# Kernel tuning notes

Hardware: AMD Instinct MI355X
Metric: run time of the kernel (lower is better)

## Reference

```python
import jax, jax.numpy as jnp
import numpy as np

HS_LIST = [1024, 2048]   # hidden_size choices
IS_LIST = [2752, 5504]   # intermediate_size choices
A_BITS = [4, 8]
W_BITS = [4, 8]


def fake_quant(t, bits):
    # symmetric per-tensor fake quantization with straight-through estimator
    qmax = 2.0 ** (bits - 1) - 1.0
    s = jnp.maximum(jnp.max(jnp.abs(t)) / qmax, 1e-8)
    q = jnp.round(t / s) * s
    return t + jax.lax.stop_gradient(q - t)


def mixed_linear(inp, W, in_sizes, out_sizes, p_in, p_out, p_a, p_w):
    """Weight-entangled mixed-precision linear: weighted sum over the
    cartesian product of (in_size, out_size, a_bit, w_bit) choices.
    W has shape [max(out_sizes), max(in_sizes)]; sub-slices are shared."""
    out_max = max(out_sizes)
    acc = jnp.zeros(inp.shape[:-1] + (out_max,), inp.dtype)
    for i, cin in enumerate(in_sizes):
        x_sub = inp[..., :cin]
        for k, ab in enumerate(A_BITS):
            xq = fake_quant(x_sub, ab)
            for j, cout in enumerate(out_sizes):
                w_sub = W[:cout, :cin]
                for l, wb in enumerate(W_BITS):
                    wq = fake_quant(w_sub, wb)
                    y = jnp.einsum('bsh,oh->bso', xq, wq)
                    y = jnp.pad(y, ((0, 0), (0, 0), (0, out_max - cout)))
                    acc = acc + (p_in[i] * p_out[j] * p_a[k] * p_w[l]) * y
    return acc


def setup_inputs() -> dict:
    key = jax.random.key(0)
    ks = jax.random.split(key, 8)
    HS, IS = max(HS_LIST), max(IS_LIST)
    return {
        'x': jax.random.normal(ks[0], (1, 1024, HS), jnp.float32),
        'p_hidden': jax.random.normal(ks[1], (2,), jnp.float32),
        'p_inter': jax.random.normal(ks[2], (2,), jnp.float32),
        'p_abit': jax.random.normal(ks[3], (2,), jnp.float32),
        'p_wbit': jax.random.normal(ks[4], (2,), jnp.float32),
        'W_gate': jax.random.normal(ks[5], (IS, HS), jnp.float32) * 0.02,
        'W_up': jax.random.normal(ks[6], (IS, HS), jnp.float32) * 0.02,
        'W_down': jax.random.normal(ks[7], (HS, IS), jnp.float32) * 0.02,
    }


def reference(x, p_hidden, p_inter, p_abit, p_wbit, W_gate, W_up, W_down):
    # mixop softmaxes the architecture parameters into mixture probabilities
    wh = jax.nn.softmax(p_hidden)
    wi = jax.nn.softmax(p_inter)
    wa = jax.nn.softmax(p_abit)
    ww = jax.nn.softmax(p_wbit)
    x_up = mixed_linear(x, W_up, HS_LIST, IS_LIST, wh, wi, wa, ww)
    x_gate = jax.nn.silu(mixed_linear(x, W_gate, HS_LIST, IS_LIST, wh, wi, wa, ww))
    h = x_gate * x_up
    # down_proj (reverse=True): input dims are intermediate, output dims hidden;
    # op list is built over (intermediate, hidden) choices, weighted in the same
    # arch-param order (hidden probs pair with the first/intermediate choice axis).
    out = mixed_linear(h, W_down, IS_LIST, HS_LIST, wh, wi, wa, ww)
    return out
```

## Files before the change

kernel.cpp:

```cpp
#include <hip/hip_runtime.h>

typedef __attribute__((ext_vector_type(8))) short short8;
typedef __attribute__((ext_vector_type(4))) float f32x4;
typedef unsigned short u16;
typedef unsigned int u32;
typedef unsigned long long u64;

#define P_WH 0
#define P_WI 2
#define P_WA 4
#define P_WW 6
#define SL_AX 8
#define SL_WUP 12
#define SL_WGATE 16
#define SL_WDOWN 20
#define SL_AH 24
#define P_SX 28
#define P_SWUP 32
#define P_SWGATE 40
#define P_SWDOWN 48
#define P_SH 56

__device__ __forceinline__ u16 f2bf(float f) {
  u32 u = __float_as_uint(f);
  u = (u + 0x7FFFu + ((u >> 16) & 1u)) >> 16;
  return (u16)u;
}
__device__ __forceinline__ float bf2f(u16 h) { return __uint_as_float(((u32)h) << 16); }
__device__ __forceinline__ float fquant(float v, float s) { return rintf(v / s) * s; }

typedef const __attribute__((address_space(1))) u32 gl_u32;
typedef __attribute__((address_space(3))) u32 lds_u32;
__device__ __forceinline__ void gload_lds16(const void* g, void* l) {
  __builtin_amdgcn_global_load_lds((gl_u32*)g, (lds_u32*)l, 16, 0, 0);
}

#define WAITVM8()  asm volatile("s_waitcnt vmcnt(8)" ::: "memory")
#define WAITVM2()  asm volatile("s_waitcnt vmcnt(2)" ::: "memory")
#define WAITVM0()  asm volatile("s_waitcnt vmcnt(0)" ::: "memory")
#define BARRIER()  asm volatile("s_barrier" ::: "memory")

__global__ void k_init(const float* ph, const float* pi, const float* pa,
                       const float* pw, float* P) {
  if (threadIdx.x == 0) {
    u32* U = (u32*)P;
    for (int i = SL_AX; i < SL_AH + 2; ++i) U[i] = 0u;
    const float* src[4] = {ph, pi, pa, pw};
    #pragma unroll
    for (int t = 0; t < 4; ++t) {
      float a = src[t][0], b = src[t][1];
      float mx = fmaxf(a, b);
      float ea = expf(a - mx), eb = expf(b - mx);
      float s = ea + eb;
      P[t * 2 + 0] = ea / s;
      P[t * 2 + 1] = eb / s;
    }
  }
}

template <bool POW2>
__device__ __forceinline__ void amax_proc(float4 d, int v, u32 magic, int C,
                                          int r0, int c0,
                                          float& m0, float& m1, float& m2, float& m3) {
  int lin = v << 2;
  int o, c;
  if (POW2) { o = lin >> 11; c = lin & 2047; }
  else {
    o = (int)(((u64)(u32)lin * magic) >> 40);
    c = lin - o * C;
  }
  float mm = fmaxf(fmaxf(fabsf(d.x), fabsf(d.y)), fmaxf(fabsf(d.z), fabsf(d.w)));
  bool rlo = o < r0, clo = c < c0;
  m0 = fmaxf(m0, (rlo && clo) ? mm : 0.f);
  m1 = fmaxf(m1, (rlo && !clo) ? mm : 0.f);
  m2 = fmaxf(m2, (!rlo && clo) ? mm : 0.f);
  m3 = fmaxf(m3, (!rlo && !clo) ? mm : 0.f);
}

template <bool POW2>
__device__ __forceinline__ void absmax_dev(const float4* __restrict__ A4,
                                           int nvec, u32 magic, int C, int r0, int c0,
                                           int slotbase, float* P, int bid, int nb) {
  float m0 = 0.f, m1 = 0.f, m2 = 0.f, m3 = 0.f;
  const int tid = threadIdx.x;
  const int step = nb * 256;
  int v = bid * 256 + tid;
  for (; v + 3 * step < nvec; v += 4 * step) {
    float4 d0 = A4[v];
    float4 d1 = A4[v + step];
    float4 d2 = A4[v + 2 * step];
    float4 d3 = A4[v + 3 * step];
    amax_proc<POW2>(d0, v,            magic, C, r0, c0, m0, m1, m2, m3);
    amax_proc<POW2>(d1, v + step,     magic, C, r0, c0, m0, m1, m2, m3);
    amax_proc<POW2>(d2, v + 2 * step, magic, C, r0, c0, m0, m1, m2, m3);
    amax_proc<POW2>(d3, v + 3 * step, magic, C, r0, c0, m0, m1, m2, m3);
  }
  for (; v < nvec; v += step) {
    float4 d0 = A4[v];
    amax_proc<POW2>(d0, v, magic, C, r0, c0, m0, m1, m2, m3);
  }
  #pragma unroll
  for (int off = 32; off > 0; off >>= 1) {
    m0 = fmaxf(m0, __shfl_xor(m0, off));
    m1 = fmaxf(m1, __shfl_xor(m1, off));
    m2 = fmaxf(m2, __shfl_xor(m2, off));
    m3 = fmaxf(m3, __shfl_xor(m3, off));
  }
  __shared__ float red[16];
  const int wave = tid >> 6;
  if ((tid & 63) == 0) {
    red[wave * 4 + 0] = m0;
    red[wave * 4 + 1] = m1;
    red[wave * 4 + 2] = m2;
    red[wave * 4 + 3] = m3;
  }
  __syncthreads();
  if (tid < 4) {
    float mm = fmaxf(fmaxf(red[tid], red[4 + tid]), fmaxf(red[8 + tid], red[12 + tid]));
    if (mm > 0.f) atomicMax((u32*)P + slotbase + tid, __float_as_uint(mm));
  }
}

__global__ __launch_bounds__(256) void k_absmax4(const float* x, const float* Wu,
                                                 const float* Wg, const float* Wd,
                                                 u32 magic5504, float* P) {
  int b = blockIdx.x;
  if (b < 256)        absmax_dev<true >((const float4*)x,  (1024 * 2048) >> 2, 0, 2048, 1024, 1024, SL_AX,    P, b,        256);
  else if (b < 768)   absmax_dev<true >((const float4*)Wu, (5504 * 2048) >> 2, 0, 2048, 2752, 1024, SL_WUP,   P, b - 256,  512);
  else if (b < 1280)  absmax_dev<true >((const float4*)Wg, (5504 * 2048) >> 2, 0, 2048, 2752, 1024, SL_WGATE, P, b - 768,  512);
  else                absmax_dev<false>((const float4*)Wd, (2048 * 5504) >> 2, magic5504, 5504, 1024, 2752, SL_WDOWN, P, b - 1280, 512);
}

__global__ void k_params1(float* P) {
  if (threadIdx.x != 0 || blockIdx.x != 0) return;
  u32* U = (u32*)P;
  float x00 = __uint_as_float(U[SL_AX + 0]);
  float x01 = __uint_as_float(U[SL_AX + 1]);
  float ax0 = x00;
  float ax1 = fmaxf(x00, x01);
  P[P_SX + 0] = fmaxf(ax0 / 7.f, 1e-8f);
  P[P_SX + 1] = fmaxf(ax0 / 127.f, 1e-8f);
  P[P_SX + 2] = fmaxf(ax1 / 7.f, 1e-8f);
  P[P_SX + 3] = fmaxf(ax1 / 127.f, 1e-8f);
  const int sl[3] = {SL_WUP, SL_WGATE, SL_WDOWN};
  const int sb[3] = {P_SWUP, P_SWGATE, P_SWDOWN};
  #pragma unroll
  for (int t = 0; t < 3; ++t) {
    float q00 = __uint_as_float(U[sl[t] + 0]);
    float q01 = __uint_as_float(U[sl[t] + 1]);
    float q10 = __uint_as_float(U[sl[t] + 2]);
    float q11 = __uint_as_float(U[sl[t] + 3]);
    float a0 = q00;
    float a1 = fmaxf(q00, q10);
    float a2 = fmaxf(q00, q01);
    float a3 = fmaxf(fmaxf(q00, q01), fmaxf(q10, q11));
    float aa[4] = {a0, a1, a2, a3};
    #pragma unroll
    for (int ij = 0; ij < 4; ++ij) {
      P[sb[t] + ij * 2 + 0] = fmaxf(aa[ij] / 7.f, 1e-8f);
      P[sb[t] + ij * 2 + 1] = fmaxf(aa[ij] / 127.f, 1e-8f);
    }
  }
}

__global__ void k_params2(float* P) {
  if (threadIdx.x != 0 || blockIdx.x != 0) return;
  u32* U = (u32*)P;
  float a0 = __uint_as_float(U[SL_AH]);
  float a1 = fmaxf(a0, __uint_as_float(U[SL_AH + 1]));
  P[P_SH + 0] = fmaxf(a0 / 7.f, 1e-8f);
  P[P_SH + 1] = fmaxf(a0 / 127.f, 1e-8f);
  P[P_SH + 2] = fmaxf(a1 / 7.f, 1e-8f);
  P[P_SH + 3] = fmaxf(a1 / 127.f, 1e-8f);
}

__device__ __forceinline__ void build_x_one(
    const float* __restrict__ src, const float* __restrict__ P,
    u16* __restrict__ Xh, u16* __restrict__ Xl,
    int Csrc, int cin0, int K, int sbx, int gid, int kpr) {
  int row = gid / kpr;
  int kc_out = (gid - row * kpr) << 3;
  int kc_log = kc_out ^ (((row >> 1) & 3) << 3);
  int i = (kc_log >= cin0) ? 1 : 0;
  int c = kc_log - i * cin0;
  float pin = P[P_WH + i];
  float wa0 = P[P_WA], wa1 = P[P_WA + 1];
  float s4 = P[sbx + i * 2], s8 = P[sbx + i * 2 + 1];
  const float* sp = src + (size_t)row * Csrc + c;
  float v[8];
  *(float4*)&v[0] = *(const float4*)sp;
  *(float4*)&v[4] = *(const float4*)(sp + 4);
  short8 hv, lv;
  #pragma unroll
  for (int e = 0; e < 8; ++e) {
    float val = pin * (wa0 * fquant(v[e], s4) + wa1 * fquant(v[e], s8));
    u16 h = f2bf(val);
    hv[e] = (short)h;
    lv[e] = (short)f2bf(val - bf2f(h));
  }
  size_t off = (size_t)row * K + kc_out;
  *(short8*)(Xh + off) = hv;
  *(short8*)(Xl + off) = lv;
}

__device__ __forceinline__ void build_w_one(
    const float* __restrict__ W, const float* __restrict__ P,
    u16* __restrict__ Wh, u16* __restrict__ Wl,
    int Csrc, int cin0, int K, int sbw, int cout0,
    int row_src, int row_store, int kc_out) {
  int kc_log = kc_out ^ (((row_store >> 1) & 3) << 3);
  int i = (kc_log >= cin0) ? 1 : 0;
  int c = kc_log - i * cin0;
  float wi0 = P[P_WI], wi1 = P[P_WI + 1];
  float ww0 = P[P_WW], ww1 = P[P_WW + 1];
  float s00 = P[sbw + i * 4 + 0];
  float s01 = P[sbw + i * 4 + 1];
  float s10 = P[sbw + i * 4 + 2];
  float s11 = P[sbw + i * 4 + 3];
  float keep0 = (row_src < cout0) ? wi0 : 0.f;
  const float* sp = W + (size_t)row_src * Csrc + c;
  float v[8];
  *(float4*)&v[0] = *(const float4*)sp;
  *(float4*)&v[4] = *(const float4*)(sp + 4);
  short8 hv, lv;
  #pragma unroll
  for (int e = 0; e < 8; ++e) {
    float w = v[e];
    float t0 = ww0 * fquant(w, s00) + ww1 * fquant(w, s01);
    float t1 = ww0 * fquant(w, s10) + ww1 * fquant(w, s11);
    float val = keep0 * t0 + wi1 * t1;
    u16 h = f2bf(val);
    hv[e] = (short)h;
    lv[e] = (short)f2bf(val - bf2f(h));
  }
  size_t off = (size_t)row_store * K + kc_out;
  *(short8*)(Wh + off) = hv;
  *(short8*)(Wl + off) = lv;
}

__global__ __launch_bounds__(256) void k_build_x(
    const float* __restrict__ src, const float* __restrict__ P,
    u16* __restrict__ Xh, u16* __restrict__ Xl,
    int rows, int Csrc, int cin0, int K, int sbx) {
  int kpr = K >> 3;
  int nch = rows * kpr;
  int gid = blockIdx.x * blockDim.x + threadIdx.x;
  if (gid >= nch) return;
  build_x_one(src, P, Xh, Xl, Csrc, cin0, K, sbx, gid, kpr);
}

__global__ __launch_bounds__(256) void k_build_w(
    const float* __restrict__ W, const float* __restrict__ P,
    u16* __restrict__ Wh, u16* __restrict__ Wl,
    int R, int Csrc, int cin0, int K, int sbw, int cout0) {
  int kpr = K >> 3;
  int nch = R * kpr;
  int gid = blockIdx.x * blockDim.x + threadIdx.x;
  if (gid >= nch) return;
  int row = gid / kpr;
  int kc_out = (gid - row * kpr) << 3;
  build_w_one(W, P, Wh, Wl, Csrc, cin0, K, sbw, cout0, row, row, kc_out);
}

__global__ __launch_bounds__(256) void k_build1(
    const float* __restrict__ x, const float* __restrict__ Wu,
    const float* __restrict__ Wg, const float* __restrict__ P,
    u16* __restrict__ X1h, u16* __restrict__ X1l,
    u16* __restrict__ Wh, u16* __restrict__ Wl) {
  int bid = blockIdx.x;
  if (bid < 1536) {
    int gid = bid * 256 + threadIdx.x;
    build_x_one(x, P, X1h, X1l, 2048, 1024, 3072, P_SX, gid, 384);
  } else {
    int gid = (bid - 1536) * 256 + threadIdx.x;
    const int nch = 5504 * 384;
    bool isg = gid >= nch;
    int g2 = isg ? gid - nch : gid;
    int row = g2 / 384;
    int kc_out = (g2 - row * 384) << 3;
    int row_store = (((row >> 4) << 5) + (row & 15)) + (isg ? 16 : 0);
    if (!isg)
      build_w_one(Wu, P, Wh, Wl, 2048, 1024, 3072, P_SWUP,   2752, row, row_store, kc_out);
    else
      build_w_one(Wg, P, Wh, Wl, 2048, 1024, 3072, P_SWGATE, 2752, row, row_store, kc_out);
  }
}

__global__ __launch_bounds__(256) void k_build2(
    const float* __restrict__ H, const float* __restrict__ Wd,
    const float* __restrict__ P,
    u16* __restrict__ X2h, u16* __restrict__ X2l,
    u16* __restrict__ Wdh, u16* __restrict__ Wdl) {
  int bid = blockIdx.x;
  if (bid < 4128) {
    int gid = bid * 256 + threadIdx.x;
    build_x_one(H, P, X2h, X2l, 5504, 2752, 8256, P_SH, gid, 1032);
  } else {
    int gid = (bid - 4128) * 256 + threadIdx.x;
    int row = gid / 1032;
    int kc_out = (gid - row * 1032) << 3;
    build_w_one(Wd, P, Wdh, Wdl, 5504, 2752, 8256, P_SWDOWN, 1024, row, row, kc_out);
  }
}

__global__ __launch_bounds__(256) void k_h(const float* __restrict__ U_,
                                           const float* __restrict__ G_,
                                           float* __restrict__ H_, float* P) {
  int nvec = (1024 * 5504) >> 2;
  int gstride = gridDim.x * blockDim.x;
  float m0 = 0.f, m1 = 0.f;
  for (int v = blockIdx.x * blockDim.x + threadIdx.x; v < nvec; v += gstride) {
    float4 u = ((const float4*)U_)[v];
    float4 g = ((const float4*)G_)[v];
    float4 h;
    h.x = u.x * (g.x / (1.f + expf(-g.x)));
    h.y = u.y * (g.y / (1.f + expf(-g.y)));
    h.z = u.z * (g.z / (1.f + expf(-g.z)));
    h.w = u.w * (g.w / (1.f + expf(-g.w)));
    ((float4*)H_)[v] = h;
    int c = (v << 2) % 5504;
    float mm = fmaxf(fmaxf(fabsf(h.x), fabsf(h.y)), fmaxf(fabsf(h.z), fabsf(h.w)));
    if (c < 2752) m0 = fmaxf(m0, mm); else m1 = fmaxf(m1, mm);
  }
  #pragma unroll
  for (int off = 32; off > 0; off >>= 1) {
    m0 = fmaxf(m0, __shfl_xor(m0, off));
    m1 = fmaxf(m1, __shfl_xor(m1, off));
  }
  if ((threadIdx.x & 63) == 0) {
    u32* slots = (u32*)P;
    if (m0 > 0.f) atomicMax(slots + SL_AH, __float_as_uint(m0));
    if (m1 > 0.f) atomicMax(slots + SL_AH + 1, __float_as_uint(m1));
  }
}

template <int MF, int NF>
__global__ __launch_bounds__(256) void k_gemm(
    const u16* __restrict__ Ah, const u16* __restrict__ Al,
    const u16* __restrict__ Bh, const u16* __restrict__ Bl,
    float* __restrict__ C0, float* __restrict__ C1, int nsplit, int ldc,
    int M, int N, int K) {
  constexpr int BM = MF * 32;
  constexpr int BN = NF * 32;
  constexpr int HALF = (2 * BM + 2 * BN) * 32;
  constexpr int nsegA = BM / 16;
  constexpr int nsegB = BN / 16;
  constexpr int NSEG = 2 * nsegA + 2 * nsegB;
  constexpr int NJ = NSEG / 4;
  static_assert(NJ == 8, "vmcnt immediates assume 8 loads per stage");
  __shared__ __align__(16) u16 S[2 * HALF];

  const int tid = threadIdx.x;
  const int wave = tid >> 6;
  const int lane = tid & 63;

  const int gx = gridDim.x;
  const int nwg = gx * gridDim.y;
  const int orig = blockIdx.y * gx + blockIdx.x;
  const int q = nwg >> 3, r = nwg & 7;
  const int xcd = orig & 7, linb = orig >> 3;
  const int swz = (xcd < r ? xcd * (q + 1) : r * (q + 1) + (xcd - r) * q) + linb;
  const int m0 = (swz % gx) * BM;
  const int n0 = (swz / gx) * BN;

  const int St = K >> 5;
  const int Z = gridDim.z;
  const int zb = St / Z, zr = St - zb * Z;
  const int z = blockIdx.z;
  const int nst = zb + ((z < zr) ? 1 : 0);
  const int k0 = (z * zb + ((z < zr) ? z : zr)) << 5;

  const int wr = wave >> 1, wc = wave & 1;
  const int lrow = lane >> 2;
  const int lcol = (lane & 3) << 3;
  const int fr = lane & 15;
  const int fq4 = (lane >> 4) << 2;
  const int kofs = (lane >> 4) << 3;

  f32x4 acc[MF][NF];
  #pragma unroll
  for (int m = 0; m < MF; ++m)
    #pragma unroll
    for (int n = 0; n < NF; ++n) acc[m][n] = (f32x4){0.f, 0.f, 0.f, 0.f};

  const u16* srcp[NJ];
  int loff[NJ];
  #pragma unroll
  for (int j = 0; j < NJ; ++j) {
    int g = j * 4 + wave;
    const u16* gb; int abase, trow, segi;
    if (g < nsegA)               { gb = Ah; abase = 0;                  trow = m0; segi = g; }
    else if (g < 2 * nsegA)      { gb = Al; abase = BM * 32;            trow = m0; segi = g - nsegA; }
    else if (g < 2 * nsegA + nsegB) { gb = Bh; abase = 2 * BM * 32;     trow = n0; segi = g - 2 * nsegA; }
    else                         { gb = Bl; abase = 2 * BM * 32 + BN * 32; trow = n0; segi = g - 2 * nsegA - nsegB; }
    srcp[j] = gb + (size_t)(trow + segi * 16 + lrow) * K + (k0 + lcol);
    loff[j] = abase + segi * 512;
  }

  int aoh[MF], aol[MF], boh[NF], bol[NF];
  #pragma unroll
  for (int m = 0; m < MF; ++m) {
    int rr = wr * (MF * 16) + m * 16 + fr;
    int idx = rr * 32 + (kofs ^ (((rr >> 1) & 3) << 3));
    aoh[m] = idx;
    aol[m] = BM * 32 + idx;
  }
  #pragma unroll
  for (int n = 0; n < NF; ++n) {
    int rr = wc * (NF * 16) + n * 16 + fr;
    int idx = rr * 32 + (kofs ^ (((rr >> 1) & 3) << 3));
    boh[n] = 2 * BM * 32 + idx;
    bol[n] = 2 * BM * 32 + BN * 32 + idx;
  }

  #define STAGE(bufo)                                           \
    { _Pragma("unroll")                                         \
      for (int j = 0; j < NJ; ++j) {                            \
        gload_lds16(srcp[j], S + (bufo) + loff[j]);             \
        srcp[j] += 32;                                          \
      } }

  #define COMPUTE(bufo)                                                         \
    { short8 afh[MF], afl[MF], bfh[NF], bfl[NF];                                \
      _Pragma("unroll")                                                         \
      for (int m = 0; m < MF; ++m) {                                            \
        afh[m] = *(const short8*)(S + (bufo) + aoh[m]);                         \
        afl[m] = *(const short8*)(S + (bufo) + aol[m]);                         \
      }                                                                         \
      _Pragma("unroll")                                                         \
      for (int n = 0; n < NF; ++n) {                                            \
        bfh[n] = *(const short8*)(S + (bufo) + boh[n]);                         \
        bfl[n] = *(const short8*)(S + (bufo) + bol[n]);                         \
      }                                                                         \
      _Pragma("unroll")                                                         \
      for (int m = 0; m < MF; ++m)                                              \
        _Pragma("unroll")                                                       \
        for (int n = 0; n < NF; ++n) {                                          \
          acc[m][n] = __builtin_amdgcn_mfma_f32_16x16x32_bf16(afh[m], bfh[n], acc[m][n], 0, 0, 0); \
          acc[m][n] = __builtin_amdgcn_mfma_f32_16x16x32_bf16(afh[m], bfl[n], acc[m][n], 0, 0, 0); \
          acc[m][n] = __builtin_amdgcn_mfma_f32_16x16x32_bf16(afl[m], bfh[n], acc[m][n], 0, 0, 0); \
        } }

  int curo = 0;
  STAGE(curo);
  for (int t = 0; t + 1 < nst; ++t) {
    STAGE(curo ^ HALF);
    WAITVM8();
    BARRIER();
    COMPUTE(curo);
    BARRIER();
    curo ^= HALF;
  }
  WAITVM0();
  BARRIER();
  COMPUTE(curo);

  #undef STAGE
  #undef COMPUTE

  float* base = (n0 < nsplit) ? C0 : C1;
  const int ncol0 = (n0 < nsplit) ? 0 : nsplit;
  float* Cz = base + (size_t)z * M * ldc;
  #pragma unroll
  for (int m = 0; m < MF; ++m) {
    #pragma unroll
    for (int n = 0; n < NF; ++n) {
      int row = m0 + wr * (MF * 16) + m * 16 + fq4;
      int col = n0 + wc * (NF * 16) + n * 16 + fr - ncol0;
      float* cp = Cz + (size_t)row * ldc + col;
      f32x4 a = acc[m][n];
      cp[0] = a[0];
      cp[(size_t)ldc] = a[1];
      cp[(size_t)2 * ldc] = a[2];
      cp[(size_t)3 * ldc] = a[3];
    }
  }
}

template <int CMODE>
__global__ __launch_bounds__(512) void k_gemm8w(
    const u16* __restrict__ Ah, const u16* __restrict__ Al,
    const u16* __restrict__ Bh, const u16* __restrict__ Bl,
    float* __restrict__ C0, float* __restrict__ C1, int nsplit, int ldc,
    int M, int N, int K) {
  constexpr int BM = 256, BN = 256;
  constexpr int HALF = (2 * BM + 2 * BN) * 32;
  constexpr int NJ = 8;
  __shared__ __align__(16) u16 S[2 * HALF];

  const int tid = threadIdx.x;
  const int wave = tid >> 6;
  const int lane = tid & 63;

  const int gx = gridDim.x;
  const int nwg = gx * gridDim.y;
  const int orig = blockIdx.y * gx + blockIdx.x;
  const int q = nwg >> 3, r = nwg & 7;
  const int xcd = orig & 7, linb = orig >> 3;
  const int swz = (xcd < r ? xcd * (q + 1) : r * (q + 1) + (xcd - r) * q) + linb;
  const int m0 = (swz % gx) * BM;
  const int n0 = (swz / gx) * BN;

  const int St = K >> 5;
  const int Z = gridDim.z;
  const int zb = St / Z, zr = St - zb * Z;
  const int z = blockIdx.z;
  const int nst = zb + ((z < zr) ? 1 : 0);
  const int k0 = (z * zb + ((z < zr) ? z : zr)) << 5;

  const int wr = wave >> 2;
  const int wc = wave & 3;
  const int lrow = lane >> 2;
  const int lcol = (lane & 3) << 3;
  const int fr = lane & 15;
  const int fq4 = (lane >> 4) << 2;
  const int kofs = (lane >> 4) << 3;
  const int kx = kofs ^ (((fr >> 1) & 3) << 3);

  f32x4 acc[8][4];
  #pragma unroll
  for (int m = 0; m < 8; ++m)
    #pragma unroll
    for (int n = 0; n < 4; ++n) acc[m][n] = (f32x4){0.f, 0.f, 0.f, 0.f};

  const u16* srcp[NJ];
  int loff[NJ];
  #pragma unroll
  for (int j = 0; j < NJ; ++j) {
    int g = j * 8 + wave;
    const u16* gb; int abase, trow, segi;
    if (g < 16)      { gb = Ah; abase = 0;         trow = m0; segi = g; }
    else if (g < 32) { gb = Al; abase = 8192;      trow = m0; segi = g - 16; }
    else if (g < 48) { gb = Bh; abase = 16384;     trow = n0; segi = g - 32; }
    else             { gb = Bl; abase = 24576;     trow = n0; segi = g - 48; }
    srcp[j] = gb + (size_t)(trow + segi * 16 + lrow) * K + (k0 + lcol);
    loff[j] = abase + segi * 512;
  }

  const int aoh0 = (wr * 128 + fr) * 32 + kx;
  const int aol0 = 8192 + aoh0;
  const int boh0 = 16384 + (wc * 64 + fr) * 32 + kx;
  const int bol0 = boh0 + 8192;

  #define ISSUE2(bufo, j0)                                             \
    { gload_lds16(srcp[j0], S + (bufo) + loff[j0]);  srcp[j0] += 32;   \
      gload_lds16(srcp[j0+1], S + (bufo) + loff[j0+1]); srcp[j0+1] += 32; }

  int curo = 0;
  ISSUE2(curo, 0); ISSUE2(curo, 2); ISSUE2(curo, 4); ISSUE2(curo, 6);

  for (int t = 0; t < nst; ++t) {
    const int nxt = curo ^ HALF;
    const bool more = (t + 1 < nst);
    if (more) { ISSUE2(nxt, 0); WAITVM2(); } else { WAITVM0(); }
    BARRIER();

    short8 bh_[4], bl_[4];
    #pragma unroll
    for (int p = 0; p < 4; ++p) {
      const int m2 = 2 * p;
      short8 a0h = *(const short8*)(S + curo + aoh0 + m2 * 512);
      short8 a0l = *(const short8*)(S + curo + aol0 + m2 * 512);
      short8 a1h = *(const short8*)(S + curo + aoh0 + (m2 + 1) * 512);
      short8 a1l = *(const short8*)(S + curo + aol0 + (m2 + 1) * 512);
      if (p == 0) {
        #pragma unroll
        for (int n = 0; n < 4; ++n) {
          bh_[n] = *(const short8*)(S + curo + boh0 + n * 512);
          bl_[n] = *(const short8*)(S + curo + bol0 + n * 512);
        }
      }
      if (more) {
        if (p == 0) { ISSUE2(nxt, 2); }
        else if (p == 1) { ISSUE2(nxt, 4); }
        else if (p == 2) { ISSUE2(nxt, 6); }
      }
      BARRIER();
      __builtin_amdgcn_s_setprio(1);
      #pragma unroll
      for (int n = 0; n < 4; ++n) {
        acc[m2][n] = __builtin_amdgcn_mfma_f32_16x16x32_bf16(a0h, bh_[n], acc[m2][n], 0, 0, 0);
        acc[m2][n] = __builtin_amdgcn_mfma_f32_16x16x32_bf16(a0h, bl_[n], acc[m2][n], 0, 0, 0);
        acc[m2][n] = __builtin_amdgcn_mfma_f32_16x16x32_bf16(a0l, bh_[n], acc[m2][n], 0, 0, 0);
        acc[m2+1][n] = __builtin_amdgcn_mfma_f32_16x16x32_bf16(a1h, bh_[n], acc[m2+1][n], 0, 0, 0);
        acc[m2+1][n] = __builtin_amdgcn_mfma_f32_16x16x32_bf16(a1h, bl_[n], acc[m2+1][n], 0, 0, 0);
        acc[m2+1][n] = __builtin_amdgcn_mfma_f32_16x16x32_bf16(a1l, bh_[n], acc[m2+1][n], 0, 0, 0);
      }
      __builtin_amdgcn_s_setprio(0);
      BARRIER();
    }
    curo ^= HALF;
  }
  #undef ISSUE2

  if (CMODE == 2) {
    float hm0 = 0.f, hm1 = 0.f;
    #pragma unroll
    for (int nn = 0; nn < 2; ++nn) {
      const int n = nn * 2;
      int lcol2 = (((n0 + wc * 64 + n * 16) >> 5) << 4) + fr;
      bool lo = lcol2 < 2752;
      #pragma unroll
      for (int m = 0; m < 8; ++m) {
        int row = m0 + wr * 128 + m * 16 + fq4;
        float* hp = C0 + (size_t)row * ldc + lcol2;
        f32x4 au = acc[m][n], ag = acc[m][n + 1];
        #pragma unroll
        for (int j = 0; j < 4; ++j) {
          float g = ag[j];
          float h = au[j] * (g / (1.f + expf(-g)));
          hp[(size_t)j * ldc] = h;
          float a = fabsf(h);
          if (lo) hm0 = fmaxf(hm0, a); else hm1 = fmaxf(hm1, a);
        }
      }
    }
    #pragma unroll
    for (int off = 32; off > 0; off >>= 1) {
      hm0 = fmaxf(hm0, __shfl_xor(hm0, off));
      hm1 = fmaxf(hm1, __shfl_xor(hm1, off));
    }
    if (lane == 0) {
      u32* slots = (u32*)C1;
      if (hm0 > 0.f) atomicMax(slots + SL_AH, __float_as_uint(hm0));
      if (hm1 > 0.f) atomicMax(slots + SL_AH + 1, __float_as_uint(hm1));
    }
  } else {
    float* Cz = (z < 4) ? (C0 + (size_t)z * M * ldc) : (C1 + (size_t)(z - 4) * M * ldc);
    #pragma unroll
    for (int m = 0; m < 8; ++m) {
      #pragma unroll
      for (int n = 0; n < 4; ++n) {
        int row = m0 + wr * 128 + m * 16 + fq4;
        int col = n0 + wc * 64 + n * 16 + fr;
        float* cp = Cz + (size_t)row * ldc + col;
        f32x4 a = acc[m][n];
        cp[0] = a[0];
        cp[(size_t)ldc] = a[1];
        cp[(size_t)2 * ldc] = a[2];
        cp[(size_t)3 * ldc] = a[3];
      }
    }
  }
}

__global__ __launch_bounds__(256) void k_reduce8(const float4* __restrict__ p0,
                                                 const float4* __restrict__ p1,
                                                 float4* __restrict__ out, int nvec) {
  int stride = gridDim.x * blockDim.x;
  for (int i = blockIdx.x * blockDim.x + threadIdx.x; i < nvec; i += stride) {
    float4 s = p0[i];
    #pragma unroll
    for (int zz = 1; zz < 4; ++zz) {
      float4 b = p0[(size_t)zz * nvec + i];
      s.x += b.x; s.y += b.y; s.z += b.z; s.w += b.w;
    }
    #pragma unroll
    for (int zz = 0; zz < 4; ++zz) {
      float4 b = p1[(size_t)zz * nvec + i];
      s.x += b.x; s.y += b.y; s.z += b.z; s.w += b.w;
    }
    out[i] = s;
  }
}

__global__ __launch_bounds__(256) void k_reduce4(const float4* __restrict__ p,
                                                 float4* __restrict__ out, int nvec) {
  int stride = gridDim.x * blockDim.x;
  for (int i = blockIdx.x * blockDim.x + threadIdx.x; i < nvec; i += stride) {
    float4 a = p[i], b = p[nvec + i], c = p[2 * nvec + i], d = p[3 * nvec + i];
    float4 o;
    o.x = ((a.x + b.x) + c.x) + d.x;
    o.y = ((a.y + b.y) + c.y) + d.y;
    o.z = ((a.z + b.z) + c.z) + d.z;
    o.w = ((a.w + b.w) + c.w) + d.w;
    out[i] = o;
  }
}

extern "C" void kernel_launch(void* const* d_in, const int* in_sizes, int n_in,
                              void* d_out, int out_size, void* d_ws, size_t ws_size,
                              hipStream_t stream) {
  const float* x  = (const float*)d_in[0];
  const float* ph = (const float*)d_in[1];
  const float* pi = (const float*)d_in[2];
  const float* pa = (const float*)d_in[3];
  const float* pw = (const float*)d_in[4];
  const float* Wg = (const float*)d_in[5];
  const float* Wu = (const float*)d_in[6];
  const float* Wd = (const float*)d_in[7];
  float* out = (float*)d_out;

  const u32 magic5504 = (u32)(((1ULL << 40) + 5503ULL) / 5504ULL);
  char* ws = (char*)d_ws;

  const size_t szX1 = (size_t)1024 * 3072 * 2;
  const size_t szWug = (size_t)11008 * 3072 * 2;
  const size_t szH = (size_t)1024 * 5504 * 4;
  const size_t szDP = (size_t)4 * 1024 * 2048 * 4;
  const size_t fused_need = 1024 + 2 * szX1 + 2 * szWug + szH + szDP;

  if (ws_size >= fused_need) {
    size_t off = 0;
    float* P = (float*)(ws + off); off += 1024;
    u16* X1h = (u16*)(ws + off); off += szX1;
    u16* X1l = (u16*)(ws + off); off += szX1;
    u16* Wh  = (u16*)(ws + off); off += szWug;
    u16* Wl  = (u16*)(ws + off); off += szWug;
    float* H = (float*)(ws + off); off += szH;
    float* DPz0 = (float*)(ws + off); off += szDP;
    u16* X2h = Wh;
    u16* X2l = Wh + (size_t)1024 * 8256;
    float* DPz1 = (float*)(Wh + (size_t)2 * 1024 * 8256);
    u16* Wdh = Wl;
    u16* Wdl = Wl + (size_t)2048 * 8256;

    k_init<<<1, 64, 0, stream>>>(ph, pi, pa, pw, P);
    k_absmax4<<<1792, 256, 0, stream>>>(x, Wu, Wg, Wd, magic5504, P);
    k_params1<<<1, 64, 0, stream>>>(P);

    k_build1<<<1536 + 16512, 256, 0, stream>>>(x, Wu, Wg, P, X1h, X1l, Wh, Wl);

    dim3 g1(1024 / 256, 11008 / 256, 1);
    k_gemm8w<2><<<g1, 512, 0, stream>>>(X1h, X1l, Wh, Wl, H, P, 5504, 5504,
                                        1024, 11008, 3072);

    k_params2<<<1, 64, 0, stream>>>(P);

    k_build2<<<4128 + 8256, 256, 0, stream>>>(H, Wd, P, X2h, X2l, Wdh, Wdl);

    dim3 g2(1024 / 256, 2048 / 256, 8);
    k_gemm8w<1><<<g2, 512, 0, stream>>>(X2h, X2l, Wdh, Wdl, DPz0, DPz1, 2048, 2048,
                                        1024, 2048, 8256);
    k_reduce8<<<2048, 256, 0, stream>>>((const float4*)DPz0, (const float4*)DPz1,
                                        (float4*)out, (1024 * 2048) / 4);
    return;
  }

  size_t off = 0;
  float* P = (float*)(ws + off); off += 1024;
  u16* X1h = (u16*)(ws + off); off += szX1;
  u16* X1l = (u16*)(ws + off); off += szX1;
  u16* Wh  = (u16*)(ws + off); off += (size_t)5504 * 3072 * 2;
  u16* Wl  = (u16*)(ws + off); off += (size_t)5504 * 3072 * 2;
  float* UP   = (float*)(ws + off); off += (size_t)1024 * 5504 * 4;
  float* GATE = (float*)(ws + off); off += (size_t)1024 * 5504 * 4;
  u16* X2h = (u16*)(ws + off); off += (size_t)1024 * 8256 * 2;
  u16* X2l = (u16*)(ws + off); off += (size_t)1024 * 8256 * 2;
  float* H = UP;
  float* DPART = UP;
  if (ws_size < off) return;

  k_init<<<1, 64, 0, stream>>>(ph, pi, pa, pw, P);
  k_absmax4<<<1792, 256, 0, stream>>>(x, Wu, Wg, Wd, magic5504, P);
  k_params1<<<1, 64, 0, stream>>>(P);

  {
    int nch = 1024 * (3072 / 8);
    k_build_x<<<(nch + 255) / 256, 256, 0, stream>>>(x, P, X1h, X1l, 1024, 2048, 1024, 3072, P_SX);
  }
  {
    int nch = 5504 * (3072 / 8);
    k_build_w<<<(nch + 255) / 256, 256, 0, stream>>>(Wu, P, Wh, Wl, 5504, 2048, 1024, 3072, P_SWUP, 2752);
  }
  dim3 g1(1024 / 128, 5504 / 128, 1);
  k_gemm<4, 4><<<g1, 256, 0, stream>>>(X1h, X1l, Wh, Wl, UP, UP, 5504, 5504, 1024, 5504, 3072);
  {
    int nch = 5504 * (3072 / 8);
    k_build_w<<<(nch + 255) / 256, 256, 0, stream>>>(Wg, P, Wh, Wl, 5504, 2048, 1024, 3072, P_SWGATE, 2752);
  }
  k_gemm<4, 4><<<g1, 256, 0, stream>>>(X1h, X1l, Wh, Wl, GATE, GATE, 5504, 5504, 1024, 5504, 3072);

  k_h<<<2048, 256, 0, stream>>>(UP, GATE, H, P);
  k_params2<<<1, 64, 0, stream>>>(P);

  {
    int nch = 1024 * (8256 / 8);
    k_build_x<<<(nch + 255) / 256, 256, 0, stream>>>(H, P, X2h, X2l, 1024, 5504, 2752, 8256, P_SH);
  }
  {
    int nch = 2048 * (8256 / 8);
    k_build_w<<<(nch + 255) / 256, 256, 0, stream>>>(Wd, P, Wh, Wl, 2048, 5504, 2752, 8256, P_SWDOWN, 1024);
  }
  dim3 g2(1024 / 128, 2048 / 128, 4);
  k_gemm<4, 4><<<g2, 256, 0, stream>>>(X2h, X2l, Wh, Wl, DPART, DPART, 2048, 2048, 1024, 2048, 8256);
  k_reduce4<<<2048, 256, 0, stream>>>((const float4*)DPART, (float4*)out, (1024 * 2048) / 4);
}
```

Baseline: 473.7 us.

## Co-launch down-proj weight build alongside first GEMM in one fused kernel

```diff
diff --git a/kernel.cpp b/kernel.cpp
--- a/kernel.cpp
+++ b/kernel.cpp
@@ -478,23 +478,19 @@
 }
 
 template <int CMODE>
-__global__ __launch_bounds__(512) void k_gemm8w(
+__device__ __forceinline__ void gemm8w_body(
     const u16* __restrict__ Ah, const u16* __restrict__ Al,
     const u16* __restrict__ Bh, const u16* __restrict__ Bl,
     float* __restrict__ C0, float* __restrict__ C1, int nsplit, int ldc,
-    int M, int N, int K) {
+    int M, int N, int K, u16* S, int orig, int gx, int nwg, int z, int Z) {
   constexpr int BM = 256, BN = 256;
   constexpr int HALF = (2 * BM + 2 * BN) * 32;
   constexpr int NJ = 8;
-  __shared__ __align__(16) u16 S[2 * HALF];
 
   const int tid = threadIdx.x;
   const int wave = tid >> 6;
   const int lane = tid & 63;
 
-  const int gx = gridDim.x;
-  const int nwg = gx * gridDim.y;
-  const int orig = blockIdx.y * gx + blockIdx.x;
   const int q = nwg >> 3, r = nwg & 7;
   const int xcd = orig & 7, linb = orig >> 3;
   const int swz = (xcd < r ? xcd * (q + 1) : r * (q + 1) + (xcd - r) * q) + linb;
@@ -502,9 +498,7 @@
   const int n0 = (swz / gx) * BN;
 
   const int St = K >> 5;
-  const int Z = gridDim.z;
   const int zb = St / Z, zr = St - zb * Z;
-  const int z = blockIdx.z;
   const int nst = zb + ((z < zr) ? 1 : 0);
   const int k0 = (z * zb + ((z < zr) ? z : zr)) << 5;
 
@@ -644,6 +638,38 @@
   }
 }
 
+template <int CMODE>
+__global__ __launch_bounds__(512) void k_gemm8w(
+    const u16* __restrict__ Ah, const u16* __restrict__ Al,
+    const u16* __restrict__ Bh, const u16* __restrict__ Bl,
+    float* __restrict__ C0, float* __restrict__ C1, int nsplit, int ldc,
+    int M, int N, int K) {
+  __shared__ __align__(16) u16 S[2 * (2 * 256 + 2 * 256) * 32];
+  int orig = blockIdx.y * gridDim.x + blockIdx.x;
+  gemm8w_body<CMODE>(Ah, Al, Bh, Bl, C0, C1, nsplit, ldc, M, N, K, S,
+                     orig, gridDim.x, gridDim.x * gridDim.y, blockIdx.z, gridDim.z);
+}
+
+__global__ __launch_bounds__(512) void k_fused1(
+    const u16* __restrict__ X1h, const u16* __restrict__ X1l,
+    const u16* __restrict__ Wh, const u16* __restrict__ Wl,
+    float* __restrict__ H, float* __restrict__ P,
+    const float* __restrict__ Wd,
+    u16* __restrict__ Wdh, u16* __restrict__ Wdl) {
+  __shared__ __align__(16) u16 S[2 * (2 * 256 + 2 * 256) * 32];
+  const int NG = 172;
+  int bid = blockIdx.x;
+  if (bid < NG) {
+    gemm8w_body<2>(X1h, X1l, Wh, Wl, H, P, 5504, 5504, 1024, 11008, 3072, S,
+                   bid, 4, NG, 0, 1);
+  } else {
+    int gid = (bid - NG) * 512 + threadIdx.x;
+    int row = gid / 1032;
+    int kc_out = (gid - row * 1032) << 3;
+    build_w_one(Wd, P, Wdh, Wdl, 5504, 2752, 8256, P_SWDOWN, 1024, row, row, kc_out);
+  }
+}
+
 __global__ __launch_bounds__(256) void k_reduce8(const float4* __restrict__ p0,
                                                  const float4* __restrict__ p1,
                                                  float4* __restrict__ out, int nvec) {
@@ -698,9 +724,11 @@
   const size_t szWug = (size_t)11008 * 3072 * 2;
   const size_t szH = (size_t)1024 * 5504 * 4;
   const size_t szDP = (size_t)4 * 1024 * 2048 * 4;
-  const size_t fused_need = 1024 + 2 * szX1 + 2 * szWug + szH + szDP;
-
-  if (ws_size >= fused_need) {
+  const size_t szWd1 = (size_t)2048 * 8256 * 2;
+  const size_t need_r15 = 1024 + 2 * szX1 + 2 * szWug + szH + szDP;
+  const size_t need_co  = need_r15 + 2 * szWd1;
+
+  if (ws_size >= need_r15) {
     size_t off = 0;
     float* P = (float*)(ws + off); off += 1024;
     u16* X1h = (u16*)(ws + off); off += szX1;
@@ -712,8 +740,9 @@
     u16* X2h = Wh;
     u16* X2l = Wh + (size_t)1024 * 8256;
     float* DPz1 = (float*)(Wh + (size_t)2 * 1024 * 8256);
-    u16* Wdh = Wl;
-    u16* Wdl = Wl + (size_t)2048 * 8256;
+    const bool colaunch = (ws_size >= need_co);
+    u16* Wdh = colaunch ? (u16*)(ws + off) : Wl;
+    u16* Wdl = colaunch ? (u16*)(ws + off + szWd1) : (Wl + (size_t)2048 * 8256);
 
     k_init<<<1, 64, 0, stream>>>(ph, pi, pa, pw, P);
     k_absmax4<<<1792, 256, 0, stream>>>(x, Wu, Wg, Wd, magic5504, P);
@@ -721,13 +750,17 @@
 
     k_build1<<<1536 + 16512, 256, 0, stream>>>(x, Wu, Wg, P, X1h, X1l, Wh, Wl);
 
-    dim3 g1(1024 / 256, 11008 / 256, 1);
-    k_gemm8w<2><<<g1, 512, 0, stream>>>(X1h, X1l, Wh, Wl, H, P, 5504, 5504,
-                                        1024, 11008, 3072);
-
-    k_params2<<<1, 64, 0, stream>>>(P);
-
-    k_build2<<<4128 + 8256, 256, 0, stream>>>(H, Wd, P, X2h, X2l, Wdh, Wdl);
+    if (colaunch) {
+      k_fused1<<<172 + 4128, 512, 0, stream>>>(X1h, X1l, Wh, Wl, H, P, Wd, Wdh, Wdl);
+      k_params2<<<1, 64, 0, stream>>>(P);
+      k_build2<<<4128, 256, 0, stream>>>(H, Wd, P, X2h, X2l, Wdh, Wdl);
+    } else {
+      dim3 g1(1024 / 256, 11008 / 256, 1);
+      k_gemm8w<2><<<g1, 512, 0, stream>>>(X1h, X1l, Wh, Wl, H, P, 5504, 5504,
+                                          1024, 11008, 3072);
+      k_params2<<<1, 64, 0, stream>>>(P);
+      k_build2<<<4128 + 8256, 256, 0, stream>>>(H, Wd, P, X2h, X2l, Wdh, Wdl);
+    }
 
     dim3 g2(1024 / 256, 2048 / 256, 8);
     k_gemm8w<1><<<g2, 512, 0, stream>>>(X2h, X2l, Wdh, Wdl, DPz0, DPz1, 2048, 2048,
```

After: 485.3 us. +2.5%, slower.
